# Kernel optimization log

Hardware: AMD Instinct MI355X
Metric: run time of the kernel (lower is better)

## Reference

```python
import jax, jax.numpy as jnp
import numpy as np

NODES_PER_GRAPH = 32
NUM_GRAPHS = 4096
N = NUM_GRAPHS * NODES_PER_GRAPH  # 131072
DEG = 8
E = N * DEG
FEAT = 10


def setup_inputs() -> dict:
    key = jax.random.key(0)
    ks = jax.random.split(key, 32)
    x = jax.random.normal(ks[0], (N, FEAT), dtype=jnp.float32)
    src = jnp.repeat(jnp.arange(N, dtype=jnp.int64), DEG)
    dst = (src // NODES_PER_GRAPH) * NODES_PER_GRAPH + jax.random.randint(
        ks[1], (E,), 0, NODES_PER_GRAPH).astype(jnp.int64)
    edge_index = jnp.stack([src, dst])  # [2, E], row0 = source j, row1 = target i
    batch = (jnp.arange(N, dtype=jnp.int64) // NODES_PER_GRAPH)

    def lin(k, fan_in, shape):
        return jax.random.normal(k, shape, dtype=jnp.float32) / np.sqrt(fan_in)

    inp = dict(x=x, edge_index=edge_index, batch=batch)
    inp['Wq'] = lin(ks[2], 32, (32, 32))
    inp['Wk'] = lin(ks[3], 32, (32, 32))
    inp['Wv'] = lin(ks[4], 32, (32, 32))
    inp['W1'] = lin(ks[5], 10, (10, 64));  inp['a1s'] = lin(ks[6], 16, (4, 16))
    inp['a1d'] = lin(ks[7], 16, (4, 16));  inp['b1'] = jnp.zeros((64,), jnp.float32)
    inp['W2'] = lin(ks[8], 64, (64, 64));  inp['a2s'] = lin(ks[9], 16, (4, 16))
    inp['a2d'] = lin(ks[10], 16, (4, 16)); inp['b2'] = jnp.zeros((64,), jnp.float32)
    inp['W3'] = lin(ks[11], 64, (64, 64)); inp['a3s'] = lin(ks[12], 16, (4, 16))
    inp['a3d'] = lin(ks[13], 16, (4, 16)); inp['b3'] = jnp.zeros((64,), jnp.float32)
    inp['W4'] = lin(ks[14], 64, (64, 64)); inp['a4s'] = lin(ks[15], 64, (1, 64))
    inp['a4d'] = lin(ks[16], 64, (1, 64)); inp['b4'] = jnp.zeros((64,), jnp.float32)
    inp['fcW'] = lin(ks[17], 64, (64, 2)); inp['fcb'] = jnp.zeros((2,), jnp.float32)
    return inp


def gat_conv(x, src, dst, W, a_s, a_d, b, heads, out_c, concat):
    n = x.shape[0]
    h = (x @ W).reshape(n, heads, out_c)                    # [N,H,C]
    e_s = jnp.einsum('nhc,hc->nh', h, a_s)
    e_d = jnp.einsum('nhc,hc->nh', h, a_d)
    e = jax.nn.leaky_relu(e_s[src] + e_d[dst], 0.2)          # [E,H]
    e_max = jax.ops.segment_max(e, dst, num_segments=n)
    e = jnp.exp(e - e_max[dst])
    denom = jax.ops.segment_sum(e, dst, num_segments=n)
    alpha = e / (denom[dst] + 1e-16)                         # softmax per target node
    msg = h[src] * alpha[:, :, None]                         # [E,H,C]
    out = jax.ops.segment_sum(msg, dst, num_segments=n)      # [N,H,C]
    out = out.reshape(n, heads * out_c) if concat else out.mean(axis=1)
    return out + b


def forward(x, edge_index, batch, Wq, Wk, Wv, W1, a1s, a1d, b1, W2, a2s, a2d, b2,
            W3, a3s, a3d, b3, W4, a4s, a4d, b4, fcW, fcb):
    n = x.shape[0]
    b = n // NODES_PER_GRAPH
    # Attention_Layer1: (b*32, 10) -> (b, 10, 32)
    att_in = x.reshape(b, NODES_PER_GRAPH, FEAT).transpose(0, 2, 1)  # [b, sl=10, 32]
    Q = att_in @ Wq
    K = att_in @ Wk
    V = att_in @ Wv
    alpha = jax.nn.softmax(jnp.einsum('bsi,bti->bst', Q, K), axis=2)
    out = jnp.einsum('bst,bti->bsi', alpha, V)               # [b, 10, 32]
    # rearrange 'b i sl -> (b sl) i' with i=10, sl=32
    xg = out.transpose(0, 2, 1).reshape(n, FEAT)             # [(b*32), 10]
    # add self-loops (PyG GATConv default)
    loops = jnp.arange(n, dtype=edge_index.dtype)
    src = jnp.concatenate([edge_index[0], loops])
    dst = jnp.concatenate([edge_index[1], loops])
    xg = jax.nn.leaky_relu(gat_conv(xg, src, dst, W1, a1s, a1d, b1, 4, 16, True), 0.01)
    xg = jax.nn.leaky_relu(gat_conv(xg, src, dst, W2, a2s, a2d, b2, 4, 16, True), 0.01)
    xg = jax.nn.leaky_relu(gat_conv(xg, src, dst, W3, a3s, a3d, b3, 4, 16, True), 0.01)
    xg = jax.nn.leaky_relu(gat_conv(xg, src, dst, W4, a4s, a4d, b4, 1, 64, True), 0.01)
    # global mean pool per graph
    sums = jax.ops.segment_sum(xg, batch, num_segments=b)
    cnts = jax.ops.segment_sum(jnp.ones((n, 1), xg.dtype), batch, num_segments=b)
    pooled = sums / cnts                                     # [b, 64]
    logits = pooled @ fcW + fcb                              # [b, 2]
    probas = jax.nn.softmax(logits, axis=1)
    return logits, probas


def reference(x, edge_index, batch, Wq, Wk, Wv, W1, a1s, a1d, b1, W2, a2s, a2d, b2,
              W3, a3s, a3d, b3, W4, a4s, a4d, b4, fcW, fcb):
    return forward(x, edge_index, batch, Wq, Wk, Wv, W1, a1s, a1d, b1, W2, a2s, a2d,
                   b2, W3, a3s, a3d, b3, W4, a4s, a4d, b4, fcW, fcb)
```

## Files before the change

kernel.cpp:

```cpp
#include <hip/hip_runtime.h>


#define NGRAPH 4096
#define EDGES  (NGRAPH * 256)
#define NT     256
#define LOG2E  1.4426950408889634f

typedef __attribute__((ext_vector_type(8))) short bf16x8;
typedef __attribute__((ext_vector_type(4))) float f32x4;
typedef __attribute__((ext_vector_type(4))) int   i32x4;

__device__ __forceinline__ unsigned f2u(float x){ union{float f;unsigned u;}c;c.f=x;return c.u; }
__device__ __forceinline__ float u2f(unsigned u){ union{unsigned u;float f;}c;c.u=u;return c.f; }

__device__ __forceinline__ void split2(float x0, float x1, unsigned& dhi, unsigned& dlo){
    const unsigned u0 = f2u(x0), u1 = f2u(x1);
    dhi = (u0 >> 16) | (u1 & 0xffff0000u);
    const float l0 = x0 - u2f(u0 & 0xffff0000u);
    const float l1 = x1 - u2f(u1 & 0xffff0000u);
    dlo = (f2u(l0) >> 16) | (f2u(l1) & 0xffff0000u);
}

__device__ __forceinline__ f32x4 mfma16(i32x4 a, i32x4 b, f32x4 c){
    return __builtin_amdgcn_mfma_f32_16x16x32_bf16(
        __builtin_bit_cast(bf16x8, a), __builtin_bit_cast(bf16x8, b), c, 0, 0, 0);
}

template<int KSTEPS>
__device__ __forceinline__ void gat_layer(
    int tid, unsigned short (*xh)[72], unsigned short (*xl)[72],
    unsigned short* hh_w, unsigned short* hl_w, float* esw, float* edw,
    const unsigned char* A8, const char* __restrict__ ws, int l,
    const float* __restrict__ b_g)
{
    const int lane = tid & 63, w = tid >> 6;
    const int n15 = lane & 15, q = lane >> 4;

    f32x4 hC0 = {0,0,0,0}, hC1 = {0,0,0,0};
    f32x4 eC0 = {0,0,0,0}, eC1 = {0,0,0,0};
#pragma unroll
    for (int ks = 0; ks < KSTEPS; ++ks){
        const unsigned short* wr = (const unsigned short*)(ws + l*16384)
                                   + (w*16 + n15)*64 + ks*32 + q*8;
        const i32x4 bh = *(const i32x4*)wr;
        const i32x4 bl = *(const i32x4*)(wr + 4096);
        const unsigned short* er = (const unsigned short*)(ws + 65536)
                                   + (l*4 + w)*2048 + n15*64 + ks*32 + q*8;
        const i32x4 eh = *(const i32x4*)er;
        const i32x4 el = *(const i32x4*)(er + 1024);

        const i32x4 a0h = *(const i32x4*)&xh[n15][ks*32 + q*8];
        const i32x4 a0l = *(const i32x4*)&xl[n15][ks*32 + q*8];
        hC0 = mfma16(a0h, bh, hC0); hC0 = mfma16(a0h, bl, hC0); hC0 = mfma16(a0l, bh, hC0);
        eC0 = mfma16(a0h, eh, eC0); eC0 = mfma16(a0h, el, eC0); eC0 = mfma16(a0l, eh, eC0);

        const i32x4 a1h = *(const i32x4*)&xh[16 + n15][ks*32 + q*8];
        const i32x4 a1l = *(const i32x4*)&xl[16 + n15][ks*32 + q*8];
        hC1 = mfma16(a1h, bh, hC1); hC1 = mfma16(a1h, bl, hC1); hC1 = mfma16(a1l, bh, hC1);
        eC1 = mfma16(a1h, eh, eC1); eC1 = mfma16(a1h, el, eC1); eC1 = mfma16(a1l, eh, eC1);
    }
    __syncthreads();

    if (n15 < 2){
        float* dst = n15 ? edw : esw;
#pragma unroll
        for (int r = 0; r < 4; ++r){
            dst[q*4 + r]      = eC0[r];
            dst[16 + q*4 + r] = eC1[r];
        }
    }

#pragma unroll
    for (int mt = 0; mt < 2; ++mt){
        const f32x4 hv = mt ? hC1 : hC0;
#pragma unroll
        for (int r = 0; r < 4; ++r){
            const float xv = hv[r];
            const unsigned u = f2u(xv);
            const float lo = xv - u2f(u & 0xffff0000u);
            hh_w[n15*40 + mt*16 + q*4 + r] = (unsigned short)(u >> 16);
            hl_w[n15*40 + mt*16 + q*4 + r] = (unsigned short)(f2u(lo) >> 16);
        }
    }

    float pf0[8], pf1[8];
    {
        float es8[8];
        *(float4*)&es8[0] = *(const float4*)&esw[q*8];
        *(float4*)&es8[4] = *(const float4*)&esw[q*8 + 4];
        const float ed0 = edw[n15], ed1 = edw[16 + n15];
        const uint2 c0 = *(const uint2*)&A8[n15*40 + q*8];
        const uint2 c1 = *(const uint2*)&A8[(16 + n15)*40 + q*8];
        float ss0 = 0.f, ss1 = 0.f;
#pragma unroll
        for (int jj = 0; jj < 8; ++jj){
            const unsigned cnt0 = ((jj < 4 ? c0.x >> (8*jj) : c0.y >> (8*(jj-4))) & 0xffu);
            const unsigned cnt1 = ((jj < 4 ? c1.x >> (8*jj) : c1.y >> (8*(jj-4))) & 0xffu);
            float e0 = es8[jj] + ed0; e0 = fmaxf(e0, 0.2f*e0);
            float e1 = es8[jj] + ed1; e1 = fmaxf(e1, 0.2f*e1);
            const float p0 = (float)cnt0 * exp2f(e0);
            const float p1 = (float)cnt1 * exp2f(e1);
            pf0[jj] = p0; ss0 += p0;
            pf1[jj] = p1; ss1 += p1;
        }
        ss0 += __shfl_xor(ss0, 16); ss0 += __shfl_xor(ss0, 32);
        ss1 += __shfl_xor(ss1, 16); ss1 += __shfl_xor(ss1, 32);
        if (q == 0){
            edw[n15]      = 1.f/(ss0 + 1e-16f);
            edw[16 + n15] = 1.f/(ss1 + 1e-16f);
        }
    }

    {
        const i32x4 bh = *(const i32x4*)&hh_w[n15*40 + q*8];
        const i32x4 bl = *(const i32x4*)&hl_w[n15*40 + q*8];
        f32x4 o0 = {0,0,0,0}, o1 = {0,0,0,0};
        i32x4 ph, pl; unsigned th, tl;
#pragma unroll
        for (int r = 0; r < 4; ++r){
            split2(pf0[2*r], pf0[2*r+1], th, tl); ph[r] = (int)th; pl[r] = (int)tl;
        }
        o0 = mfma16(ph, bh, o0); o0 = mfma16(ph, bl, o0); o0 = mfma16(pl, bh, o0);
#pragma unroll
        for (int r = 0; r < 4; ++r){
            split2(pf1[2*r], pf1[2*r+1], th, tl); ph[r] = (int)th; pl[r] = (int)tl;
        }
        o1 = mfma16(ph, bh, o1); o1 = mfma16(ph, bl, o1); o1 = mfma16(pl, bh, o1);

        const float bv = __ldg(b_g + w*16 + n15);
#pragma unroll
        for (int mt = 0; mt < 2; ++mt){
            const f32x4 ov = mt ? o1 : o0;
#pragma unroll
            for (int r = 0; r < 4; ++r){
                const int row = mt*16 + q*4 + r;
                float v = ov[r] * edw[row] + bv;
                v = fmaxf(v, 0.01f*v);
                const unsigned u = f2u(v);
                const float lo = v - u2f(u & 0xffff0000u);
                xh[row][w*16 + n15] = (unsigned short)(u >> 16);
                xl[row][w*16 + n15] = (unsigned short)(f2u(lo) >> 16);
            }
        }
    }
}

__global__ __launch_bounds__(NT) void gnn_fused(
    const float* __restrict__ x, const int* __restrict__ edge_index,
    const float* __restrict__ Wq, const float* __restrict__ Wk, const float* __restrict__ Wv,
    const float* __restrict__ b1, const float* __restrict__ b2,
    const float* __restrict__ b3, const float* __restrict__ b4,
    const float* __restrict__ fcW, const float* __restrict__ fcb,
    const char* __restrict__ ws, float* __restrict__ out)
{
    __shared__ __align__(16) unsigned short xap[2][32][72];
    __shared__ __align__(16) unsigned short hT[4][2][16][40];
    __shared__ __align__(16) float es_l[4][32];
    __shared__ __align__(16) float ed_l[4][32];
    __shared__ __align__(16) unsigned char A8[32*40];

    const int g = blockIdx.x, tid = threadIdx.x;
    const int w = tid >> 6;
    int* A32 = (int*)&xap[0][0][0];
    float* scr = (float*)&hT[0][0][0][0];
    float* xin = scr;
    float* qkv = scr + 384;
    float* sc  = scr + 1374;

    for (int idx = tid; idx < 1024; idx += NT) A32[idx] = 0;
    for (int idx = tid; idx < 320; idx += NT)
        xin[(idx/10)*12 + (idx%10)] = x[g*320 + idx];
    __syncthreads();

    {
        const int* dstp = edge_index + EDGES + g*256;
        atomicAdd(&A32[(dstp[tid] & 31)*32 + (tid >> 3)], 1);
        if (tid < 32) atomicAdd(&A32[tid*33], 1);
    }
    for (int idx = tid; idx < 960; idx += NT){
        const int mat = idx/320, r = idx - mat*320, s = r >> 5, i = r & 31;
        const float* Wsrc = (mat == 0) ? Wq : ((mat == 1) ? Wk : Wv);
        float acc = 0.f;
#pragma unroll
        for (int mm = 0; mm < 32; ++mm) acc += xin[mm*12 + s]*__ldg(Wsrc + mm*32 + i);
        qkv[mat*330 + s*33 + i] = acc;
    }
    __syncthreads();

    if (tid < 100){
        const int s = tid/10, t = tid - 10*(tid/10);
        const float* qs = qkv + s*33;
        const float* kt = qkv + 330 + t*33;
        float acc = 0.f;
#pragma unroll
        for (int i2 = 0; i2 < 32; ++i2) acc += qs[i2]*kt[i2];
        sc[s*11 + t] = acc;
    }
    __syncthreads();

    {
        const int i = tid >> 3, j4 = (tid & 7)*4;
        const int4 v = *(const int4*)&A32[i*32 + j4];
        *(unsigned*)&A8[i*40 + j4] =
            (unsigned)v.x | ((unsigned)v.y << 8) | ((unsigned)v.z << 16) | ((unsigned)v.w << 24);
    }
    if (tid < 10){
        float* row = sc + tid*11;
        float m = row[0];
#pragma unroll
        for (int t = 1; t < 10; ++t) m = fmaxf(m, row[t]);
        float ssum = 0.f;
#pragma unroll
        for (int t = 0; t < 10; ++t){ const float e = __expf(row[t]-m); row[t] = e; ssum += e; }
        const float inv = 1.f/ssum;
#pragma unroll
        for (int t = 0; t < 10; ++t) row[t] *= inv;
    }
    __syncthreads();

    for (int idx = tid; idx < 2048; idx += NT){
        const int i = idx >> 6, s = idx & 63;
        float acc = 0.f;
        if (s < 10){
#pragma unroll
            for (int t = 0; t < 10; ++t) acc += sc[s*11 + t]*qkv[660 + t*33 + i];
        }
        const unsigned u = f2u(acc);
        const float lo = acc - u2f(u & 0xffff0000u);
        xap[0][i][s] = (unsigned short)(u >> 16);
        xap[1][i][s] = (unsigned short)(f2u(lo) >> 16);
    }
    __syncthreads();

    unsigned short (*xh)[72] = xap[0];
    unsigned short (*xl)[72] = xap[1];
    unsigned short* hh_w = &hT[w][0][0][0];
    unsigned short* hl_w = &hT[w][1][0][0];
    float* esw = es_l[w];
    float* edw = ed_l[w];
    gat_layer<1>(tid, xh, xl, hh_w, hl_w, esw, edw, A8, ws, 0, b1);
    __syncthreads();
    gat_layer<2>(tid, xh, xl, hh_w, hl_w, esw, edw, A8, ws, 1, b2);
    __syncthreads();
    gat_layer<2>(tid, xh, xl, hh_w, hl_w, esw, edw, A8, ws, 2, b3);
    __syncthreads();
    gat_layer<2>(tid, xh, xl, hh_w, hl_w, esw, edw, A8, ws, 3, b4);
    __syncthreads();

    if (tid < 64){
        float acc = 0.f;
#pragma unroll
        for (int n = 0; n < 32; ++n)
            acc += u2f(((unsigned)xap[0][n][tid]) << 16) + u2f(((unsigned)xap[1][n][tid]) << 16);
        const float p = acc*(1.f/32.f);
        float c0 = p*__ldg(fcW + 2*tid);
        float c1 = p*__ldg(fcW + 2*tid + 1);
#pragma unroll
        for (int off = 32; off > 0; off >>= 1){
            c0 += __shfl_down(c0, off);
            c1 += __shfl_down(c1, off);
        }
        if (tid == 0){
            const float l0 = c0 + __ldg(fcb), l1 = c1 + __ldg(fcb + 1);
            const float m = fmaxf(l0, l1);
            const float e0 = __expf(l0 - m), e1 = __expf(l1 - m);
            const float inv = 1.f/(e0 + e1);
            out[2*g] = l0;
            out[2*g + 1] = l1;
            out[2*NGRAPH + 2*g] = e0*inv;
            out[2*NGRAPH + 2*g + 1] = e1*inv;
        }
    }
}

__global__ void prep(
    const float* __restrict__ W1, const float* __restrict__ W2,
    const float* __restrict__ W3, const float* __restrict__ W4,
    const float* __restrict__ a1s, const float* __restrict__ a1d,
    const float* __restrict__ a2s, const float* __restrict__ a2d,
    const float* __restrict__ a3s, const float* __restrict__ a3d,
    const float* __restrict__ a4s, const float* __restrict__ a4d,
    char* __restrict__ ws)
{
    const int b = blockIdx.x, tid = threadIdx.x;
    const float* Wl[4] = {W1, W2, W3, W4};
    const int Kl[4] = {10, 64, 64, 64};
    if (b < 32){
        const int l = b >> 3;
        const float* W = Wl[l];
        const int K = Kl[l];
        unsigned short* hi = (unsigned short*)(ws + l*16384);
        unsigned short* lo = hi + 4096;
        const int base = (b & 7)*512;
        for (int idx = base + tid; idx < base + 512; idx += NT){
            const int n = idx >> 6, k = idx & 63;
            const float v = (k < K) ? __ldg(W + k*64 + n) : 0.f;
            const unsigned u = f2u(v);
            const float lof = v - u2f(u & 0xffff0000u);
            hi[idx] = (unsigned short)(u >> 16);
            lo[idx] = (unsigned short)(f2u(lof) >> 16);
        }
    } else {
        const int l = b - 32;
        const float* W = Wl[l];
        const int K = Kl[l];
        const float* asp[4] = {a1s, a2s, a3s, a4s};
        const float* adp[4] = {a1d, a2d, a3d, a4d};
        const int C = (l < 3) ? 16 : 64;
        unsigned short* base = (unsigned short*)(ws + 65536);
        for (int idx = tid; idx < 4096; idx += NT){
            const int wv = idx >> 10, rem = idx & 1023, n = rem >> 6, k = rem & 63;
            float val = 0.f;
            if (n < 2 && k < K){
                const int hh = (l < 3) ? wv : 0;
                const float* av = n ? adp[l] : asp[l];
                float s = 0.f;
                for (int c = 0; c < C; ++c)
                    s += __ldg(W + k*64 + hh*C + c) * __ldg(av + hh*C + c);
                val = s * LOG2E;
            }
            const unsigned u = f2u(val);
            const float lof = val - u2f(u & 0xffff0000u);
            base[(l*4 + wv)*2048 + n*64 + k] = (unsigned short)(u >> 16);
            base[(l*4 + wv)*2048 + 1024 + n*64 + k] = (unsigned short)(f2u(lof) >> 16);
        }
    }
}

extern "C" void kernel_launch(void* const* d_in, const int* in_sizes, int n_in,
                              void* d_out, int out_size, void* d_ws, size_t ws_size,
                              hipStream_t stream) {
    (void)in_sizes; (void)n_in; (void)ws_size; (void)out_size;
    prep<<<36, NT, 0, stream>>>(
        (const float*)d_in[6], (const float*)d_in[10], (const float*)d_in[14], (const float*)d_in[18],
        (const float*)d_in[7], (const float*)d_in[8],
        (const float*)d_in[11], (const float*)d_in[12],
        (const float*)d_in[15], (const float*)d_in[16],
        (const float*)d_in[19], (const float*)d_in[20],
        (char*)d_ws);
    gnn_fused<<<NGRAPH, NT, 0, stream>>>(
        (const float*)d_in[0], (const int*)d_in[1],
        (const float*)d_in[3], (const float*)d_in[4], (const float*)d_in[5],
        (const float*)d_in[9], (const float*)d_in[13], (const float*)d_in[17], (const float*)d_in[21],
        (const float*)d_in[22], (const float*)d_in[23],
        (const char*)d_ws, (float*)d_out);
}
```

Before: 226.3 us.

## Move QKV attention prologue onto split-bf16 MFMA and pack adjacency counts directly

The per-graph self-attention prologue (Q/K/V projections, scores, softmax and the weighted sum over V) is moved from scalar FP32 loops onto 16x16x32 bf16 MFMAs. Operands are split into hi/lo bf16 pairs to keep near-FP32 accuracy, the Wq/Wk/Wv weights are pre-split in the prep kernel, and the softmax uses wave shuffles. The adjacency counts are accumulated straight into a byte-packed layout with shifted atomics, which drops the 32-bit count matrix and its separate packing pass. The attention-logit weights for all heads are now packed into one tile per layer, and each wave extracts its own head's columns. This trims the scalar work and barriers in the prologue, at the cost of more zero-padding code and a three-term split-bf16 approximation.

```diff
diff --git a/kernel.cpp b/kernel.cpp
--- a/kernel.cpp
+++ b/kernel.cpp
@@ -30,7 +30,7 @@
 __device__ __forceinline__ void gat_layer(
     int tid, unsigned short (*xh)[72], unsigned short (*xl)[72],
     unsigned short* hh_w, unsigned short* hl_w, float* esw, float* edw,
-    const unsigned char* A8, const char* __restrict__ ws, int l,
+    const unsigned int* Ap, const char* __restrict__ ws, int l,
     const float* __restrict__ b_g)
 {
     const int lane = tid & 63, w = tid >> 6;
@@ -44,8 +44,8 @@
                                    + (w*16 + n15)*64 + ks*32 + q*8;
         const i32x4 bh = *(const i32x4*)wr;
         const i32x4 bl = *(const i32x4*)(wr + 4096);
-        const unsigned short* er = (const unsigned short*)(ws + 65536)
-                                   + (l*4 + w)*2048 + n15*64 + ks*32 + q*8;
+        const unsigned short* er = (const unsigned short*)(ws + 65536 + l*4096)
+                                   + n15*64 + ks*32 + q*8;
         const i32x4 eh = *(const i32x4*)er;
         const i32x4 el = *(const i32x4*)(er + 1024);
 
@@ -61,8 +61,8 @@
     }
     __syncthreads();
 
-    if (n15 < 2){
-        float* dst = n15 ? edw : esw;
+    if (n15 == 2*w || n15 == 2*w + 1){
+        float* dst = (n15 & 1) ? edw : esw;
 #pragma unroll
         for (int r = 0; r < 4; ++r){
             dst[q*4 + r]      = eC0[r];
@@ -89,8 +89,8 @@
         *(float4*)&es8[0] = *(const float4*)&esw[q*8];
         *(float4*)&es8[4] = *(const float4*)&esw[q*8 + 4];
         const float ed0 = edw[n15], ed1 = edw[16 + n15];
-        const uint2 c0 = *(const uint2*)&A8[n15*40 + q*8];
-        const uint2 c1 = *(const uint2*)&A8[(16 + n15)*40 + q*8];
+        const uint2 c0 = make_uint2(Ap[n15*9 + 2*q], Ap[n15*9 + 2*q + 1]);
+        const uint2 c1 = make_uint2(Ap[(16+n15)*9 + 2*q], Ap[(16+n15)*9 + 2*q + 1]);
         float ss0 = 0.f, ss1 = 0.f;
 #pragma unroll
         for (int jj = 0; jj < 8; ++jj){
@@ -147,7 +147,6 @@
 
 __global__ __launch_bounds__(NT) void gnn_fused(
     const float* __restrict__ x, const int* __restrict__ edge_index,
-    const float* __restrict__ Wq, const float* __restrict__ Wk, const float* __restrict__ Wv,
     const float* __restrict__ b1, const float* __restrict__ b2,
     const float* __restrict__ b3, const float* __restrict__ b4,
     const float* __restrict__ fcW, const float* __restrict__ fcb,
@@ -157,78 +156,145 @@
     __shared__ __align__(16) unsigned short hT[4][2][16][40];
     __shared__ __align__(16) float es_l[4][32];
     __shared__ __align__(16) float ed_l[4][32];
-    __shared__ __align__(16) unsigned char A8[32*40];
+    __shared__ __align__(16) unsigned int Ap[32*9];
 
     const int g = blockIdx.x, tid = threadIdx.x;
-    const int w = tid >> 6;
-    int* A32 = (int*)&xap[0][0][0];
-    float* scr = (float*)&hT[0][0][0][0];
-    float* xin = scr;
-    float* qkv = scr + 384;
-    float* sc  = scr + 1374;
-
-    for (int idx = tid; idx < 1024; idx += NT) A32[idx] = 0;
-    for (int idx = tid; idx < 320; idx += NT)
-        xin[(idx/10)*12 + (idx%10)] = x[g*320 + idx];
+    const int lane = tid & 63, w = tid >> 6;
+    const int n15 = lane & 15, q = lane >> 4;
+
+    unsigned short* r0 = &xap[0][0][0];
+    unsigned short* r1 = &hT[0][0][0][0];
+
+    for (int idx = tid; idx < 288; idx += NT) Ap[idx] = 0u;
+    for (int idx = tid; idx < 320; idx += NT){
+        const int m = idx / 10, s = idx - 10*m;
+        const float v = x[g*320 + idx];
+        const unsigned u = f2u(v);
+        const float lo = v - u2f(u & 0xffff0000u);
+        r0[0   + s*40 + m] = (unsigned short)(u >> 16);
+        r0[640 + s*40 + m] = (unsigned short)(f2u(lo) >> 16);
+    }
+    if (tid < 192){
+        const int s = 10 + (tid >> 5), m = tid & 31;
+        r0[0   + s*40 + m] = 0;
+        r0[640 + s*40 + m] = 0;
+    }
     __syncthreads();
 
     {
         const int* dstp = edge_index + EDGES + g*256;
-        atomicAdd(&A32[(dstp[tid] & 31)*32 + (tid >> 3)], 1);
-        if (tid < 32) atomicAdd(&A32[tid*33], 1);
-    }
-    for (int idx = tid; idx < 960; idx += NT){
-        const int mat = idx/320, r = idx - mat*320, s = r >> 5, i = r & 31;
-        const float* Wsrc = (mat == 0) ? Wq : ((mat == 1) ? Wk : Wv);
-        float acc = 0.f;
-#pragma unroll
-        for (int mm = 0; mm < 32; ++mm) acc += xin[mm*12 + s]*__ldg(Wsrc + mm*32 + i);
-        qkv[mat*330 + s*33 + i] = acc;
-    }
-    __syncthreads();
-
-    if (tid < 100){
-        const int s = tid/10, t = tid - 10*(tid/10);
-        const float* qs = qkv + s*33;
-        const float* kt = qkv + 330 + t*33;
-        float acc = 0.f;
-#pragma unroll
-        for (int i2 = 0; i2 < 32; ++i2) acc += qs[i2]*kt[i2];
-        sc[s*11 + t] = acc;
-    }
-    __syncthreads();
-
-    {
-        const int i = tid >> 3, j4 = (tid & 7)*4;
-        const int4 v = *(const int4*)&A32[i*32 + j4];
-        *(unsigned*)&A8[i*40 + j4] =
-            (unsigned)v.x | ((unsigned)v.y << 8) | ((unsigned)v.z << 16) | ((unsigned)v.w << 24);
-    }
-    if (tid < 10){
-        float* row = sc + tid*11;
-        float m = row[0];
-#pragma unroll
-        for (int t = 1; t < 10; ++t) m = fmaxf(m, row[t]);
-        float ssum = 0.f;
-#pragma unroll
-        for (int t = 0; t < 10; ++t){ const float e = __expf(row[t]-m); row[t] = e; ssum += e; }
-        const float inv = 1.f/ssum;
-#pragma unroll
-        for (int t = 0; t < 10; ++t) row[t] *= inv;
-    }
-    __syncthreads();
-
-    for (int idx = tid; idx < 2048; idx += NT){
-        const int i = idx >> 6, s = idx & 63;
-        float acc = 0.f;
-        if (s < 10){
-#pragma unroll
-            for (int t = 0; t < 10; ++t) acc += sc[s*11 + t]*qkv[660 + t*33 + i];
-        }
-        const unsigned u = f2u(acc);
-        const float lo = acc - u2f(u & 0xffff0000u);
-        xap[0][i][s] = (unsigned short)(u >> 16);
-        xap[1][i][s] = (unsigned short)(f2u(lo) >> 16);
+        const int i = dstp[tid] & 31, j = tid >> 3;
+        atomicAdd(&Ap[i*9 + (j >> 2)], 1u << (8*(j & 3)));
+        if (tid < 32) atomicAdd(&Ap[tid*9 + (tid >> 2)], 1u << (8*(tid & 3)));
+    }
+    if (w < 3){
+        const unsigned short* wb = (const unsigned short*)(ws + 81920 + w*4096);
+        const i32x4 ah = *(const i32x4*)&r0[0   + n15*40 + q*8];
+        const i32x4 al = *(const i32x4*)&r0[640 + n15*40 + q*8];
+        f32x4 C0 = {0,0,0,0}, C1 = {0,0,0,0};
+#pragma unroll
+        for (int nt = 0; nt < 2; ++nt){
+            const i32x4 bh = *(const i32x4*)&wb[(nt*16 + n15)*32 + q*8];
+            const i32x4 bl = *(const i32x4*)&wb[1024 + (nt*16 + n15)*32 + q*8];
+            f32x4 acc = nt ? C1 : C0;
+            acc = mfma16(ah, bh, acc); acc = mfma16(ah, bl, acc); acc = mfma16(al, bh, acc);
+            if (nt) C1 = acc; else C0 = acc;
+        }
+        if (w < 2){
+            const int base = (w == 0) ? 1280 : 2560;
+#pragma unroll
+            for (int nt = 0; nt < 2; ++nt){
+                const f32x4 cv = nt ? C1 : C0;
+                const int i = nt*16 + n15;
+#pragma unroll
+                for (int r = 0; r < 4; ++r){
+                    const int s = q*4 + r;
+                    const float v = cv[r];
+                    const unsigned u = f2u(v);
+                    const float lo = v - u2f(u & 0xffff0000u);
+                    r0[base + s*40 + i]       = (unsigned short)(u >> 16);
+                    r0[base + 640 + s*40 + i] = (unsigned short)(f2u(lo) >> 16);
+                }
+            }
+        } else {
+#pragma unroll
+            for (int nt = 0; nt < 2; ++nt){
+                const f32x4 cv = nt ? C1 : C0;
+                const int i = nt*16 + n15;
+#pragma unroll
+                for (int r = 0; r < 4; ++r){
+                    const int t = q*4 + r;
+                    const float v = cv[r];
+                    const unsigned u = f2u(v);
+                    const float lo = v - u2f(u & 0xffff0000u);
+                    r1[0    + i*40 + t] = (unsigned short)(u >> 16);
+                    r1[1280 + i*40 + t] = (unsigned short)(f2u(lo) >> 16);
+                }
+            }
+        }
+    } else {
+        const int plane = lane >> 5, row = lane & 31;
+        unsigned short* dst = &r1[plane*1280 + row*40 + 16];
+#pragma unroll
+        for (int k = 0; k < 8; ++k) *(unsigned*)&dst[2*k] = 0u;
+    }
+    __syncthreads();
+
+    if (w == 0){
+        const i32x4 ah = *(const i32x4*)&r0[1280 + n15*40 + q*8];
+        const i32x4 al = *(const i32x4*)&r0[1920 + n15*40 + q*8];
+        const i32x4 bh = *(const i32x4*)&r0[2560 + n15*40 + q*8];
+        const i32x4 bl = *(const i32x4*)&r0[3200 + n15*40 + q*8];
+        f32x4 Sc = {0,0,0,0};
+        Sc = mfma16(ah, bh, Sc); Sc = mfma16(ah, bl, Sc); Sc = mfma16(al, bh, Sc);
+        const bool valid = (n15 < 10);
+#pragma unroll
+        for (int r = 0; r < 4; ++r){
+            float v = valid ? Sc[r] : -1e30f;
+            float m = v;
+            m = fmaxf(m, __shfl_xor(m, 1)); m = fmaxf(m, __shfl_xor(m, 2));
+            m = fmaxf(m, __shfl_xor(m, 4)); m = fmaxf(m, __shfl_xor(m, 8));
+            float p = valid ? exp2f((Sc[r] - m)*LOG2E) : 0.f;
+            float s = p;
+            s += __shfl_xor(s, 1); s += __shfl_xor(s, 2);
+            s += __shfl_xor(s, 4); s += __shfl_xor(s, 8);
+            const float sp = p / s;
+            const int srow = q*4 + r;
+            const unsigned u = f2u(sp);
+            const float lo = sp - u2f(u & 0xffff0000u);
+            r1[2560 + srow*40 + n15] = (unsigned short)(u >> 16);
+            r1[3200 + srow*40 + n15] = (unsigned short)(f2u(lo) >> 16);
+            r1[2560 + srow*40 + 16 + n15] = 0;
+            r1[3200 + srow*40 + 16 + n15] = 0;
+        }
+    }
+    __syncthreads();
+
+    if (w < 2){
+        const i32x4 ah = *(const i32x4*)&r1[2560 + n15*40 + q*8];
+        const i32x4 al = *(const i32x4*)&r1[3200 + n15*40 + q*8];
+        const i32x4 bh = *(const i32x4*)&r1[0    + (w*16 + n15)*40 + q*8];
+        const i32x4 bl = *(const i32x4*)&r1[1280 + (w*16 + n15)*40 + q*8];
+        f32x4 O = {0,0,0,0};
+        O = mfma16(ah, bh, O); O = mfma16(ah, bl, O); O = mfma16(al, bh, O);
+        const int ig = w*16 + n15;
+#pragma unroll
+        for (int r = 0; r < 4; ++r){
+            const int s = q*4 + r;
+            if (s < 10){
+                const float v = O[r];
+                const unsigned u = f2u(v);
+                const float lo = v - u2f(u & 0xffff0000u);
+                xap[0][ig][s] = (unsigned short)(u >> 16);
+                xap[1][ig][s] = (unsigned short)(f2u(lo) >> 16);
+            }
+        }
+    } else {
+        const int lane2 = tid & 127;
+        const int plane = lane2 >> 6, row = (lane2 >> 1) & 31, half = lane2 & 1;
+        unsigned short* dst = &xap[plane][row][10 + half*27];
+#pragma unroll
+        for (int c = 0; c < 27; ++c) dst[c] = 0;
     }
     __syncthreads();
 
@@ -238,13 +304,13 @@
     unsigned short* hl_w = &hT[w][1][0][0];
     float* esw = es_l[w];
     float* edw = ed_l[w];
-    gat_layer<1>(tid, xh, xl, hh_w, hl_w, esw, edw, A8, ws, 0, b1);
-    __syncthreads();
-    gat_layer<2>(tid, xh, xl, hh_w, hl_w, esw, edw, A8, ws, 1, b2);
-    __syncthreads();
-    gat_layer<2>(tid, xh, xl, hh_w, hl_w, esw, edw, A8, ws, 2, b3);
-    __syncthreads();
-    gat_layer<2>(tid, xh, xl, hh_w, hl_w, esw, edw, A8, ws, 3, b4);
+    gat_layer<1>(tid, xh, xl, hh_w, hl_w, esw, edw, Ap, ws, 0, b1);
+    __syncthreads();
+    gat_layer<2>(tid, xh, xl, hh_w, hl_w, esw, edw, Ap, ws, 1, b2);
+    __syncthreads();
+    gat_layer<2>(tid, xh, xl, hh_w, hl_w, esw, edw, Ap, ws, 2, b3);
+    __syncthreads();
+    gat_layer<2>(tid, xh, xl, hh_w, hl_w, esw, edw, Ap, ws, 3, b4);
     __syncthreads();
 
     if (tid < 64){
@@ -280,6 +346,8 @@
     const float* __restrict__ a2s, const float* __restrict__ a2d,
     const float* __restrict__ a3s, const float* __restrict__ a3d,
     const float* __restrict__ a4s, const float* __restrict__ a4d,
+    const float* __restrict__ Wq, const float* __restrict__ Wk,
+    const float* __restrict__ Wv,
     char* __restrict__ ws)
 {
     const int b = blockIdx.x, tid = threadIdx.x;
@@ -300,20 +368,20 @@
             hi[idx] = (unsigned short)(u >> 16);
             lo[idx] = (unsigned short)(f2u(lof) >> 16);
         }
-    } else {
+    } else if (b < 36){
         const int l = b - 32;
         const float* W = Wl[l];
         const int K = Kl[l];
         const float* asp[4] = {a1s, a2s, a3s, a4s};
         const float* adp[4] = {a1d, a2d, a3d, a4d};
         const int C = (l < 3) ? 16 : 64;
-        unsigned short* base = (unsigned short*)(ws + 65536);
-        for (int idx = tid; idx < 4096; idx += NT){
-            const int wv = idx >> 10, rem = idx & 1023, n = rem >> 6, k = rem & 63;
+        unsigned short* basep = (unsigned short*)(ws + 65536 + l*4096);
+        for (int idx = tid; idx < 1024; idx += NT){
+            const int n = idx >> 6, k = idx & 63;
             float val = 0.f;
-            if (n < 2 && k < K){
-                const int hh = (l < 3) ? wv : 0;
-                const float* av = n ? adp[l] : asp[l];
+            if (n < 8 && k < K){
+                const int hh = (l < 3) ? (n >> 1) : 0;
+                const float* av = (n & 1) ? adp[l] : asp[l];
                 float s = 0.f;
                 for (int c = 0; c < C; ++c)
                     s += __ldg(W + k*64 + hh*C + c) * __ldg(av + hh*C + c);
@@ -321,8 +389,21 @@
             }
             const unsigned u = f2u(val);
             const float lof = val - u2f(u & 0xffff0000u);
-            base[(l*4 + wv)*2048 + n*64 + k] = (unsigned short)(u >> 16);
-            base[(l*4 + wv)*2048 + 1024 + n*64 + k] = (unsigned short)(f2u(lof) >> 16);
+            basep[idx]        = (unsigned short)(u >> 16);
+            basep[1024 + idx] = (unsigned short)(f2u(lof) >> 16);
+        }
+    } else {
+        const int mat = b - 36;
+        const float* W = (mat == 0) ? Wq : ((mat == 1) ? Wk : Wv);
+        unsigned short* hi = (unsigned short*)(ws + 81920 + mat*4096);
+        unsigned short* lo = hi + 1024;
+        for (int idx = tid; idx < 1024; idx += NT){
+            const int i = idx >> 5, m = idx & 31;
+            const float v = __ldg(W + m*32 + i);
+            const unsigned u = f2u(v);
+            const float lof = v - u2f(u & 0xffff0000u);
+            hi[idx] = (unsigned short)(u >> 16);
+            lo[idx] = (unsigned short)(f2u(lof) >> 16);
         }
     }
 }
@@ -331,16 +412,16 @@
                               void* d_out, int out_size, void* d_ws, size_t ws_size,
                               hipStream_t stream) {
     (void)in_sizes; (void)n_in; (void)ws_size; (void)out_size;
-    prep<<<36, NT, 0, stream>>>(
+    prep<<<39, NT, 0, stream>>>(
         (const float*)d_in[6], (const float*)d_in[10], (const float*)d_in[14], (const float*)d_in[18],
         (const float*)d_in[7], (const float*)d_in[8],
         (const float*)d_in[11], (const float*)d_in[12],
         (const float*)d_in[15], (const float*)d_in[16],
         (const float*)d_in[19], (const float*)d_in[20],
+        (const float*)d_in[3], (const float*)d_in[4], (const float*)d_in[5],
         (char*)d_ws);
     gnn_fused<<<NGRAPH, NT, 0, stream>>>(
         (const float*)d_in[0], (const int*)d_in[1],
-        (const float*)d_in[3], (const float*)d_in[4], (const float*)d_in[5],
         (const float*)d_in[9], (const float*)d_in[13], (const float*)d_in[17], (const float*)d_in[21],
         (const float*)d_in[22], (const float*)d_in[23],
         (const char*)d_ws, (float*)d_out);
```

After: 203.1 us. -10.2%, faster.
